# Kernel tuning notes

Hardware: AMD Instinct MI355X
Metric: run time of the kernel (lower is better)

The kernel has to match this reference:

```python
import jax, jax.numpy as jnp
import numpy as np

EMBED = 512; HEADS = 16; WIN = 8; SHIFT = 4

def _rel_pos_index(Wh, Ww):
    # WindowMSA.double_step_seq + transpose-sum + flip(1)
    seq1 = np.arange(0, (2 * Ww - 1) * Wh, 2 * Ww - 1)
    seq2 = np.arange(0, Ww)
    coords = (seq1[:, None] + seq2[None, :]).reshape(1, -1)
    idx = coords + coords.T            # (Wh*Ww, Wh*Ww)
    return idx[:, ::-1].copy()

def _attn_mask(H_pad, W_pad, win, shift, nf):
    # static (trace-time) shifted-window mask, values in {0, -100}
    img = np.zeros((H_pad, W_pad))
    cnt = 0
    for h in (slice(0, -win), slice(-win, -shift), slice(-shift, None)):
        for w in (slice(0, -win), slice(-win, -shift), slice(-shift, None)):
            img[h, w] = cnt
            cnt += 1
    mw = img.reshape(H_pad // win, win, W_pad // win, win).transpose(0, 2, 1, 3).reshape(-1, win * win)
    am = mw[:, None, :] - mw[:, :, None]
    am = np.where(am != 0, -100.0, 0.0)
    return np.tile(am, (1, 1, nf))     # (nW, N, nf*N)

def setup_inputs():
    key = jax.random.key(0)
    ks = jax.random.split(key, 8)
    B, H, W, C, nf = 8, 128, 128, EMBED, 2
    s = 0.02
    return {
        'q': jax.random.normal(ks[0], (B, H * W, C), jnp.float32),
        'kv': jax.random.normal(ks[1], (B, nf, H * W, C), jnp.float32),
        'H': H, 'W': W,
        'rpb_table': jax.random.normal(ks[2], ((2 * WIN - 1) ** 2, HEADS), jnp.float32) * s,
        'Wq': jax.random.normal(ks[3], (C, C), jnp.float32) * s,
        'bq': jnp.zeros((C,), jnp.float32),
        'Wkv': jax.random.normal(ks[4], (C, 2 * C), jnp.float32) * s,
        'bkv': jnp.zeros((2 * C,), jnp.float32),
        'Wo': jax.random.normal(ks[5], (C, C), jnp.float32) * s,
        'bo': jnp.zeros((C,), jnp.float32),
    }

def reference(q, kv, H, W, rpb_table, Wq, bq, Wkv, bkv, Wo, bo):
    B, L, C = q.shape
    nf = kv.shape[1]
    win, shift, heads = WIN, SHIFT, HEADS
    hd = C // heads
    scale = hd ** -0.5
    pad_b = (-H) % win
    pad_r = (-W) % win
    x = q.reshape(B, H, W, C)
    kvx = kv.reshape(B * nf, H, W, C)
    x = jnp.pad(x, ((0, 0), (0, pad_b), (0, pad_r), (0, 0)))
    kvx = jnp.pad(kvx, ((0, 0), (0, pad_b), (0, pad_r), (0, 0)))
    Hp, Wp = H + pad_b, W + pad_r
    nh, nw = Hp // win, Wp // win
    if shift > 0:
        x = jnp.roll(x, (-shift, -shift), (1, 2))
        kvx = jnp.roll(kvx, (-shift, -shift), (1, 2))
        mask = jnp.asarray(_attn_mask(Hp, Wp, win, shift, nf), q.dtype)
    else:
        mask = None
    Nq = win * win
    Nk = nf * Nq
    # window partition: (B, Hp, Wp, C) -> (B*nh*nw, Nq, C)
    qw = x.reshape(B, nh, win, nw, win, C).transpose(0, 1, 3, 2, 4, 5).reshape(B * nh * nw, Nq, C)
    # kv: (B*nf, Hp, Wp, C) -> (B*nh*nw, nf*Nq, C)
    kvw = kvx.reshape(B, nf, nh, win, nw, win, C).transpose(0, 2, 4, 1, 3, 5, 6).reshape(B * nh * nw, Nk, C)
    Bw = qw.shape[0]
    qh = (qw @ Wq + bq).reshape(Bw, Nq, heads, hd).transpose(0, 2, 1, 3) * scale
    kvp = (kvw @ Wkv + bkv).reshape(Bw, Nk, 2, heads, hd).transpose(2, 0, 3, 1, 4)
    kh, vh = kvp[0], kvp[1]
    attn = jnp.einsum('bhqd,bhkd->bhqk', qh, kh)
    rpi = jnp.asarray(_rel_pos_index(win, win).reshape(-1))
    rpb = rpb_table[rpi].reshape(Nq, Nq, heads).transpose(2, 0, 1)  # (heads, Nq, Nq)
    attn = attn + jnp.tile(rpb, (1, 1, nf))[None]
    if mask is not None:
        nW = mask.shape[0]
        attn = (attn.reshape(Bw // nW, nW, heads, Nq, Nk) + mask[None, :, None]).reshape(Bw, heads, Nq, Nk)
    attn = jax.nn.softmax(attn, axis=-1)
    ow = jnp.einsum('bhqk,bhkd->bqhd', attn, vh).reshape(Bw, Nq, C)
    ow = ow @ Wo + bo
    # window reverse
    x = ow.reshape(B, nh, nw, win, win, C).transpose(0, 1, 3, 2, 4, 5).reshape(B, Hp, Wp, C)
    if shift > 0:
        x = jnp.roll(x, (shift, shift), (1, 2))
    x = x[:, :H, :W, :].reshape(B, H * W, C)
    return x
```

## Files before the change

kernel.cpp:

```cpp
#include <hip/hip_runtime.h>

typedef unsigned short ushort_t;
typedef short bf16x8 __attribute__((ext_vector_type(8)));
typedef float f32x4 __attribute__((ext_vector_type(4)));

#define MFMA16(a, b, c) __builtin_amdgcn_mfma_f32_16x16x32_bf16(a, b, c, 0, 0, 0)

static __device__ __forceinline__ float bf2f(ushort_t u) {
  union { unsigned int i; float f; } v;
  v.i = ((unsigned int)u) << 16;
  return v.f;
}
static __device__ __forceinline__ ushort_t f2bf(float f) {
  union { float f; unsigned int i; } v;
  v.f = f;
  unsigned int u = v.i;
  u = u + 0x7fffu + ((u >> 16) & 1u);
  return (ushort_t)(u >> 16);
}
static __device__ __forceinline__ unsigned int cvtpk(float lo, float hi) {
  unsigned int r;
  asm("v_cvt_pk_bf16_f32 %0, %1, %2" : "=v"(r) : "v"(lo), "v"(hi));
  return r;
}
static __device__ __forceinline__ void gload16(const void* g, void* l) {
  __builtin_amdgcn_global_load_lds((const __attribute__((address_space(1))) void*)g,
                                   (__attribute__((address_space(3))) void*)l,
                                   16, 0, 0);
}

__global__ void ws_sentinel(float* out, unsigned long long ws) {
  if (blockIdx.x == 0 && threadIdx.x == 0)
    out[0] = 1.0e6f * (1.0f + (float)(ws >> 23));
}

__global__ __launch_bounds__(256) void wtrans3(const float* __restrict__ Wq,
                                               const float* __restrict__ Wkv,
                                               const float* __restrict__ Wo,
                                               ushort_t* __restrict__ WqT,
                                               ushort_t* __restrict__ WkvT,
                                               ushort_t* __restrict__ WoT) {
  int idx = blockIdx.x * 256 + threadIdx.x;
  if (idx < 262144) {
    int r = idx >> 9, c = idx & 511;
    WqT[c * 512 + r] = f2bf(Wq[idx]);
  } else if (idx < 786432) {
    int i = idx - 262144;
    int r = i >> 10, c = i & 1023;
    WkvT[c * 512 + r] = f2bf(Wkv[i]);
  } else if (idx < 1048576) {
    int i = idx - 786432;
    int r = i >> 9, c = i & 511;
    WoT[c * 512 + r] = f2bf(Wo[i]);
  }
}

template <bool AF32, bool CF32>
__global__ __launch_bounds__(256, 2) void gemm_bt(const void* __restrict__ Av,
                                                  const ushort_t* __restrict__ Bt,
                                                  const float* __restrict__ bias,
                                                  void* __restrict__ Cv,
                                                  int N, int Nt, float cscale) {
  constexpr int K = 512;
  __shared__ __align__(16) unsigned char As[AF32 ? 128 * 32 * 4 : 128 * 32 * 2];
  __shared__ __align__(16) unsigned char Bs[128 * 32 * 2];
  const int t = threadIdx.x;
  const int l = t & 63;
  const int w = t >> 6;
  const int w32 = w * 32;
  const int wr = w >> 1, wc = w & 1;
  const int lrow = l & 15;
  const int g = l >> 4;

  const int bid = blockIdx.x;
  const int xcd = bid & 7;
  const int slot = bid >> 3;
  const int mt = xcd + 8 * (slot / Nt);
  const int nt = slot % Nt;
  const long m0 = (long)mt * 128;
  const int n0 = nt * 128;

  const int arow = l >> 3;
  const int acol = ((16 * (l & 7)) ^ ((arow & 7) << 4)) >> 2;
  const int brow = l >> 2;
  const int bcol = ((16 * (l & 3)) ^ ((brow & 3) << 4)) >> 1;

  const f32x4 fz = {0.f, 0.f, 0.f, 0.f};
  f32x4 acc[4][4];
#pragma unroll
  for (int i = 0; i < 4; i++)
#pragma unroll
    for (int j = 0; j < 4; j++) acc[i][j] = fz;

  for (int kk = 0; kk < K; kk += 32) {
    __syncthreads();
    if constexpr (AF32) {
#pragma unroll
      for (int i = 0; i < 4; i++) {
        const float* gp = (const float*)Av + (m0 + w32 + i * 8 + arow) * (long)K + kk + acol;
        gload16(gp, &As[(w32 + i * 8) * 128]);
      }
    } else {
#pragma unroll
      for (int i = 0; i < 2; i++) {
        const ushort_t* gp = (const ushort_t*)Av + (m0 + w32 + i * 16 + brow) * (long)K + kk + bcol;
        gload16(gp, &As[(w32 + i * 16) * 64]);
      }
    }
#pragma unroll
    for (int i = 0; i < 2; i++) {
      const ushort_t* gp = Bt + (long)(n0 + w32 + i * 16 + brow) * K + kk + bcol;
      gload16(gp, &Bs[(w32 + i * 16) * 64]);
    }
    __syncthreads();

    bf16x8 af[4], bfr[4];
    if constexpr (AF32) {
#pragma unroll
      for (int mi = 0; mi < 4; mi++) {
        const int aR = wr * 64 + mi * 16 + lrow;
        const int s = (aR & 7) << 4;
        const int c0 = g * 32;
        f32x4 x = *(const f32x4*)&As[aR * 128 + (c0 ^ s)];
        f32x4 y = *(const f32x4*)&As[aR * 128 + ((c0 + 16) ^ s)];
        union { unsigned int u[4]; bf16x8 v; } r;
        r.u[0] = cvtpk(x[0], x[1]);
        r.u[1] = cvtpk(x[2], x[3]);
        r.u[2] = cvtpk(y[0], y[1]);
        r.u[3] = cvtpk(y[2], y[3]);
        af[mi] = r.v;
      }
    } else {
#pragma unroll
      for (int mi = 0; mi < 4; mi++) {
        const int aR = wr * 64 + mi * 16 + lrow;
        af[mi] = *(const bf16x8*)&As[aR * 64 + ((g * 16) ^ ((aR & 3) << 4))];
      }
    }
#pragma unroll
    for (int ni = 0; ni < 4; ni++) {
      const int bR = wc * 64 + ni * 16 + lrow;
      bfr[ni] = *(const bf16x8*)&Bs[bR * 64 + ((g * 16) ^ ((bR & 3) << 4))];
    }
#pragma unroll
    for (int mi = 0; mi < 4; mi++)
#pragma unroll
      for (int ni = 0; ni < 4; ni++)
        acc[mi][ni] = MFMA16(af[mi], bfr[ni], acc[mi][ni]);
  }

#pragma unroll
  for (int mi = 0; mi < 4; mi++) {
    const long row0 = m0 + wr * 64 + mi * 16 + (l >> 4) * 4;
#pragma unroll
    for (int ni = 0; ni < 4; ni++) {
      const int col = n0 + wc * 64 + ni * 16 + lrow;
      const float bv = bias[col];
      if constexpr (CF32) {
#pragma unroll
        for (int r = 0; r < 4; r++)
          ((float*)Cv)[(row0 + r) * N + col] = (acc[mi][ni][r] + bv) * cscale;
      } else {
#pragma unroll
        for (int r = 0; r < 4; r += 2) {
          const float a0 = (acc[mi][ni][r] + bv) * cscale;
          const float a1 = (acc[mi][ni][r + 1] + bv) * cscale;
          const unsigned int pk = cvtpk(a0, a1);
          ((ushort_t*)Cv)[(row0 + r) * N + col] = (ushort_t)(pk & 0xffffu);
          ((ushort_t*)Cv)[(row0 + r + 1) * N + col] = (ushort_t)(pk >> 16);
        }
      }
    }
  }
}

__global__ __launch_bounds__(256, 1) void attn_k(const ushort_t* __restrict__ Qp,
                                                 const ushort_t* __restrict__ KVp,
                                                 const float* __restrict__ rpbt,
                                                 ushort_t* __restrict__ Ao) {
  __shared__ ushort_t P[64 * 136];
  __shared__ ushort_t Ks[128 * 32];
  __shared__ ushort_t Vt[32 * 136];
  __shared__ float Ltab[225];
  const int t = threadIdx.x;
  const int l = t & 63;
  const int w = t >> 6;
  const int wnd = blockIdx.x;
  const int h = blockIdx.y;
  const int b = wnd >> 8;
  const int wh = (wnd >> 4) & 15;
  const int ww = wnd & 15;

  const int lrow = l & 15;
  const int lq = l >> 4;
  const int lk = lq * 8;

  auto qrow = [&](int q) -> long {
    int i = q >> 3, j = q & 7;
    int ho = (wh * 8 + i + 4) & 127;
    int wo = (ww * 8 + j + 4) & 127;
    return (long)((b << 14) + (ho << 7) + wo);
  };
  auto kvrow = [&](int kp) -> long {
    int f = kp >> 6, m = kp & 63;
    int i = m >> 3, j = m & 7;
    int ho = (wh * 8 + i + 4) & 127;
    int wo = (ww * 8 + j + 4) & 127;
    return (long)(((b * 2 + f) << 14) + (ho << 7) + wo);
  };
  auto cnt_of = [&](int m) -> int {
    int hr = wh * 8 + (m >> 3), wr2 = ww * 8 + (m & 7);
    int rh = hr < 120 ? 0 : (hr < 124 ? 1 : 2);
    int rw = wr2 < 120 ? 0 : (wr2 < 124 ? 1 : 2);
    return rh * 3 + rw;
  };
  auto cvec = [](int m) -> int { return 15 * (m >> 3) + (m & 7); };

#pragma unroll
  for (int i = 0; i < 2; i++) {
    const int row = w * 32 + i * 16 + (l >> 2);
    const ushort_t* gp = KVp + kvrow(row) * 1024 + h * 32 + (l & 3) * 8;
    gload16(gp, Ks + (w * 32 + i * 16) * 32);
  }
  {
    const int vkp = t & 127;
    const int vdh = t >> 7;
    const ushort_t* vsrc = KVp + kvrow(vkp) * 1024 + 512 + h * 32 + vdh * 16;
    bf16x8 v0 = *(const bf16x8*)(vsrc);
    bf16x8 v1 = *(const bf16x8*)(vsrc + 8);
#pragma unroll
    for (int d = 0; d < 8; d++) {
      Vt[(vdh * 16 + d) * 136 + vkp] = (ushort_t)v0[d];
      Vt[(vdh * 16 + 8 + d) * 136 + vkp] = (ushort_t)v1[d];
    }
  }
  for (int i = t; i < 225; i += 256) Ltab[i] = rpbt[i * 16 + h];

  bf16x8 af = *(const bf16x8*)(Qp + qrow(w * 16 + lrow) * 512 + h * 32 + lk);

  int ck[8], lidx[8];
#pragma unroll
  for (int ni = 0; ni < 8; ni++) {
    const int k63 = (ni * 16 + lrow) & 63;
    ck[ni] = cnt_of(k63);
    lidx[ni] = cvec(63 - k63);
  }
  int cq4[4], cqv4[4];
#pragma unroll
  for (int r = 0; r < 4; r++) {
    const int q = w * 16 + lq * 4 + r;
    cq4[r] = cnt_of(q);
    cqv4[r] = cvec(q);
  }

  __syncthreads();

  const f32x4 fz = {0.f, 0.f, 0.f, 0.f};
  f32x4 s[8];
#pragma unroll
  for (int ni = 0; ni < 8; ni++) s[ni] = fz;
#pragma unroll
  for (int ni = 0; ni < 8; ni++) {
    bf16x8 kf = *(const bf16x8*)&Ks[(ni * 16 + lrow) * 32 + lk];
    s[ni] = MFMA16(af, kf, s[ni]);
  }

  float inv4[4];
#pragma unroll
  for (int r = 0; r < 4; r++) {
    float mx = -3.0e38f;
#pragma unroll
    for (int ni = 0; ni < 8; ni++) {
      float v = s[ni][r] + Ltab[cqv4[r] + lidx[ni]];
      if (ck[ni] != cq4[r]) v -= 100.f;
      s[ni][r] = v;
      mx = fmaxf(mx, v);
    }
    mx = fmaxf(mx, __shfl_xor(mx, 1));
    mx = fmaxf(mx, __shfl_xor(mx, 2));
    mx = fmaxf(mx, __shfl_xor(mx, 4));
    mx = fmaxf(mx, __shfl_xor(mx, 8));
    float sum = 0.f;
#pragma unroll
    for (int ni = 0; ni < 8; ni++) {
      float p = __expf(s[ni][r] - mx);
      s[ni][r] = p;
      sum += p;
    }
    sum += __shfl_xor(sum, 1);
    sum += __shfl_xor(sum, 2);
    sum += __shfl_xor(sum, 4);
    sum += __shfl_xor(sum, 8);
    inv4[r] = 1.f / sum;
    const int q = w * 16 + lq * 4 + r;
#pragma unroll
    for (int ni = 0; ni < 8; ni += 2) {
      const unsigned int pk = cvtpk(s[ni][r], s[ni + 1][r]);
      P[q * 136 + ni * 16 + lrow] = (ushort_t)(pk & 0xffffu);
      P[q * 136 + (ni + 1) * 16 + lrow] = (ushort_t)(pk >> 16);
    }
  }


  f32x4 o[2] = {fz, fz};
#pragma unroll
  for (int ks = 0; ks < 4; ks++) {
    bf16x8 pf = *(const bf16x8*)&P[(w * 16 + lrow) * 136 + ks * 32 + lk];
#pragma unroll
    for (int ni = 0; ni < 2; ni++) {
      bf16x8 vf = *(const bf16x8*)&Vt[(ni * 16 + lrow) * 136 + ks * 32 + lk];
      o[ni] = MFMA16(pf, vf, o[ni]);
    }
  }

#pragma unroll
  for (int ni = 0; ni < 2; ni++)
#pragma unroll
    for (int r = 0; r < 4; r += 2) {
      const unsigned int pk = cvtpk(o[ni][r] * inv4[r], o[ni][r + 1] * inv4[r + 1]);
      const int q0 = w * 16 + lq * 4 + r;
      Ao[qrow(q0) * 512 + h * 32 + ni * 16 + lrow] = (ushort_t)(pk & 0xffffu);
      Ao[qrow(q0 + 1) * 512 + h * 32 + ni * 16 + lrow] = (ushort_t)(pk >> 16);
    }
}

extern "C" void kernel_launch(void* const* d_in, const int* in_sizes, int n_in,
                              void* d_out, int out_size, void* d_ws, size_t ws_size,
                              hipStream_t stream) {
  (void)in_sizes; (void)n_in; (void)out_size;
  const float* q    = (const float*)d_in[0];
  const float* kv   = (const float*)d_in[1];
  const float* rpbt = (const float*)d_in[4];
  const float* Wq   = (const float*)d_in[5];
  const float* bq   = (const float*)d_in[6];
  const float* Wkv  = (const float*)d_in[7];
  const float* bkv  = (const float*)d_in[8];
  const float* Wo   = (const float*)d_in[9];
  const float* bo   = (const float*)d_in[10];
  float* out = (float*)d_out;

  const size_t QB  = 16384ULL * 512;
  const size_t KVB = 32768ULL * 1024;
  const size_t per_b_bytes = (QB + QB + KVB) * 2;
  const size_t fixed_bytes = (512ULL*512 + 512ULL*1024 + 512ULL*512) * 2;
  const size_t needed1 = fixed_bytes + per_b_bytes;

  if (ws_size < needed1) {
    ws_sentinel<<<dim3(1), 64, 0, stream>>>(out, (unsigned long long)ws_size);
    return;
  }

  int nbc = 8;
  while (nbc > 1 && fixed_bytes + (size_t)nbc * per_b_bytes > ws_size) nbc >>= 1;

  char* ws = (char*)d_ws;
  ushort_t* WqT  = (ushort_t*)ws;
  ushort_t* WkvT = WqT + 512 * 512;
  ushort_t* WoT  = WkvT + 512 * 1024;
  ushort_t* Qp   = (ushort_t*)(ws + fixed_bytes);
  ushort_t* Ao   = Qp + (size_t)nbc * QB;
  ushort_t* KVp  = Ao + (size_t)nbc * QB;

  wtrans3<<<dim3(4096), 256, 0, stream>>>(Wq, Wkv, Wo, WqT, WkvT, WoT);

  const float scale = 0.17677669529663687f;
  for (int c = 0; c < 8 / nbc; ++c) {
    const size_t b0 = (size_t)c * nbc;
    const int MtQ = nbc * 128;
    const int MtKV = nbc * 256;
    gemm_bt<true, false><<<dim3(MtQ * 4), 256, 0, stream>>>(q + b0 * QB, WqT, bq,
                                                            Qp, 512, 4, scale);
    gemm_bt<true, false><<<dim3(MtKV * 8), 256, 0, stream>>>(kv + b0 * KVB / 2, WkvT,
                                                             bkv, KVp, 1024, 8, 1.0f);
    attn_k<<<dim3(nbc * 256, 16), 256, 0, stream>>>(Qp, KVp, rpbt, Ao);
    gemm_bt<false, true><<<dim3(MtQ * 4), 256, 0, stream>>>(Ao, WoT, bo,
                                                            out + b0 * QB, 512, 4, 1.0f);
  }
}
```

Before: 1.008 ms.

## Double-buffer GEMM LDS tiles with register-prefetched A and convert-on-store

Restructures the projection GEMM main loop into a two-stage LDS double buffer. The next-next A tile is prefetched into registers and B is staged by async global-to-LDS loads, with explicit waitcnt and barriers, so memory latency overlaps the MFMA work. For fp32 A inputs, the bf16 conversion now happens once when writing to LDS instead of on every fragment read, which halves the A LDS footprint. The cost is more registers and tighter manual synchronisation, which could lower occupancy.

```diff
diff --git a/kernel.cpp b/kernel.cpp
--- a/kernel.cpp
+++ b/kernel.cpp
@@ -62,8 +62,9 @@
                                                   void* __restrict__ Cv,
                                                   int N, int Nt, float cscale) {
   constexpr int K = 512;
-  __shared__ __align__(16) unsigned char As[AF32 ? 128 * 32 * 4 : 128 * 32 * 2];
-  __shared__ __align__(16) unsigned char Bs[128 * 32 * 2];
+  constexpr int NT = K / 32;
+  __shared__ __align__(16) ushort_t As[2][128 * 32];
+  __shared__ __align__(16) ushort_t Bs[2][128 * 32];
   const int t = threadIdx.x;
   const int l = t & 63;
   const int w = t >> 6;
@@ -80,10 +81,19 @@
   const long m0 = (long)mt * 128;
   const int n0 = nt * 128;
 
-  const int arow = l >> 3;
-  const int acol = ((16 * (l & 7)) ^ ((arow & 7) << 4)) >> 2;
-  const int brow = l >> 2;
-  const int bcol = ((16 * (l & 3)) ^ ((brow & 3) << 4)) >> 1;
+  const int srow = l >> 2;
+  const int sseg = l & 3;
+  const int swz = ((srow & 3) << 3);
+  const int bcol = (sseg * 8) ^ swz;
+  const int acolw = (sseg * 8) ^ swz;
+
+  auto stageB = [&](int buf, int kk) {
+#pragma unroll
+    for (int i = 0; i < 2; i++) {
+      const ushort_t* gp = Bt + (long)(n0 + w32 + i * 16 + srow) * K + kk + bcol;
+      gload16(gp, &Bs[buf][(w32 + i * 16) * 32]);
+    }
+  };
 
   const f32x4 fz = {0.f, 0.f, 0.f, 0.f};
   f32x4 acc[4][4];
@@ -92,61 +102,105 @@
 #pragma unroll
     for (int j = 0; j < 4; j++) acc[i][j] = fz;
 
-  for (int kk = 0; kk < K; kk += 32) {
+  {
+#pragma unroll
+    for (int tt = 0; tt < 2; tt++) {
+      const int kk = tt * 32;
+      if constexpr (AF32) {
+#pragma unroll
+        for (int i = 0; i < 2; i++) {
+          const float* gp = (const float*)Av + (m0 + w32 + i * 16 + srow) * (long)K + kk + sseg * 8;
+          f32x4 x = *(const f32x4*)gp;
+          f32x4 y = *(const f32x4*)(gp + 4);
+          union { unsigned int u[4]; bf16x8 v; } r;
+          r.u[0] = cvtpk(x[0], x[1]);
+          r.u[1] = cvtpk(x[2], x[3]);
+          r.u[2] = cvtpk(y[0], y[1]);
+          r.u[3] = cvtpk(y[2], y[3]);
+          *(bf16x8*)&As[tt][(w32 + i * 16 + srow) * 32 + acolw] = r.v;
+        }
+      } else {
+#pragma unroll
+        for (int i = 0; i < 2; i++) {
+          const ushort_t* gp = (const ushort_t*)Av + (m0 + w32 + i * 16 + srow) * (long)K + kk + sseg * 8;
+          bf16x8 x = *(const bf16x8*)gp;
+          *(bf16x8*)&As[tt][(w32 + i * 16 + srow) * 32 + acolw] = x;
+        }
+      }
+      stageB(tt, kk);
+    }
     __syncthreads();
-    if constexpr (AF32) {
-#pragma unroll
-      for (int i = 0; i < 4; i++) {
-        const float* gp = (const float*)Av + (m0 + w32 + i * 8 + arow) * (long)K + kk + acol;
-        gload16(gp, &As[(w32 + i * 8) * 128]);
+  }
+
+  for (int ts = 0; ts < NT; ++ts) {
+    const int cur = ts & 1;
+    const bool pre = (ts + 2 < NT);
+
+    f32x4 axf[4];
+    bf16x8 axb[2];
+    if (pre) {
+      const int kk = (ts + 2) * 32;
+      if constexpr (AF32) {
+#pragma unroll
+        for (int i = 0; i < 2; i++) {
+          const float* gp = (const float*)Av + (m0 + w32 + i * 16 + srow) * (long)K + kk + sseg * 8;
+          axf[2 * i] = *(const f32x4*)gp;
+          axf[2 * i + 1] = *(const f32x4*)(gp + 4);
+        }
+      } else {
+#pragma unroll
+        for (int i = 0; i < 2; i++) {
+          const ushort_t* gp = (const ushort_t*)Av + (m0 + w32 + i * 16 + srow) * (long)K + kk + sseg * 8;
+          axb[i] = *(const bf16x8*)gp;
+        }
       }
-    } else {
-#pragma unroll
-      for (int i = 0; i < 2; i++) {
-        const ushort_t* gp = (const ushort_t*)Av + (m0 + w32 + i * 16 + brow) * (long)K + kk + bcol;
-        gload16(gp, &As[(w32 + i * 16) * 64]);
-      }
-    }
-#pragma unroll
-    for (int i = 0; i < 2; i++) {
-      const ushort_t* gp = Bt + (long)(n0 + w32 + i * 16 + brow) * K + kk + bcol;
-      gload16(gp, &Bs[(w32 + i * 16) * 64]);
-    }
-    __syncthreads();
+    }
 
     bf16x8 af[4], bfr[4];
-    if constexpr (AF32) {
-#pragma unroll
-      for (int mi = 0; mi < 4; mi++) {
-        const int aR = wr * 64 + mi * 16 + lrow;
-        const int s = (aR & 7) << 4;
-        const int c0 = g * 32;
-        f32x4 x = *(const f32x4*)&As[aR * 128 + (c0 ^ s)];
-        f32x4 y = *(const f32x4*)&As[aR * 128 + ((c0 + 16) ^ s)];
-        union { unsigned int u[4]; bf16x8 v; } r;
-        r.u[0] = cvtpk(x[0], x[1]);
-        r.u[1] = cvtpk(x[2], x[3]);
-        r.u[2] = cvtpk(y[0], y[1]);
-        r.u[3] = cvtpk(y[2], y[3]);
-        af[mi] = r.v;
-      }
-    } else {
-#pragma unroll
-      for (int mi = 0; mi < 4; mi++) {
-        const int aR = wr * 64 + mi * 16 + lrow;
-        af[mi] = *(const bf16x8*)&As[aR * 64 + ((g * 16) ^ ((aR & 3) << 4))];
-      }
+#pragma unroll
+    for (int mi = 0; mi < 4; mi++) {
+      const int aR = wr * 64 + mi * 16 + lrow;
+      af[mi] = *(const bf16x8*)&As[cur][aR * 32 + ((g * 8) ^ ((aR & 3) << 3))];
     }
 #pragma unroll
     for (int ni = 0; ni < 4; ni++) {
       const int bR = wc * 64 + ni * 16 + lrow;
-      bfr[ni] = *(const bf16x8*)&Bs[bR * 64 + ((g * 16) ^ ((bR & 3) << 4))];
+      bfr[ni] = *(const bf16x8*)&Bs[cur][bR * 32 + ((g * 8) ^ ((bR & 3) << 3))];
     }
 #pragma unroll
     for (int mi = 0; mi < 4; mi++)
 #pragma unroll
       for (int ni = 0; ni < 4; ni++)
         acc[mi][ni] = MFMA16(af[mi], bfr[ni], acc[mi][ni]);
+
+    __builtin_amdgcn_sched_barrier(0);
+    __builtin_amdgcn_s_barrier();
+    __builtin_amdgcn_sched_barrier(0);
+
+    if (pre) {
+      if constexpr (AF32) {
+#pragma unroll
+        for (int i = 0; i < 2; i++) {
+          union { unsigned int u[4]; bf16x8 v; } r;
+          r.u[0] = cvtpk(axf[2 * i][0], axf[2 * i][1]);
+          r.u[1] = cvtpk(axf[2 * i][2], axf[2 * i][3]);
+          r.u[2] = cvtpk(axf[2 * i + 1][0], axf[2 * i + 1][1]);
+          r.u[3] = cvtpk(axf[2 * i + 1][2], axf[2 * i + 1][3]);
+          *(bf16x8*)&As[cur][(w32 + i * 16 + srow) * 32 + acolw] = r.v;
+        }
+      } else {
+#pragma unroll
+        for (int i = 0; i < 2; i++)
+          *(bf16x8*)&As[cur][(w32 + i * 16 + srow) * 32 + acolw] = axb[i];
+      }
+      stageB(cur, (ts + 2) * 32);
+      asm volatile("s_waitcnt vmcnt(2) lgkmcnt(0)" ::: "memory");
+    } else {
+      asm volatile("s_waitcnt vmcnt(0) lgkmcnt(0)" ::: "memory");
+    }
+    __builtin_amdgcn_sched_barrier(0);
+    __builtin_amdgcn_s_barrier();
+    __builtin_amdgcn_sched_barrier(0);
   }
 
 #pragma unroll
```

New measurement: 989.8 us. No clear change (-1.9%).
